# Optimization experiments

Measured on AMD Instinct MI355X. Metric: run time of the kernel, lower is better.

The kernel has to match this reference:

```python
import jax, jax.numpy as jnp
import numpy as np

B, T, K = 1024, 512, 64
START, STOP = K - 2, K - 1
NEG = -10000.0


def setup_inputs() -> dict:
    key = jax.random.key(0)
    k1, k2, k3, k4 = jax.random.split(key, 4)
    feats = jax.random.normal(k1, (B, T, K), dtype=jnp.float32)
    lengths = jax.random.randint(k2, (B,), 1, T + 1)  # valid seq lengths in [1, T]
    tags = jax.random.randint(k3, (B, T), 0, K)
    transitions = jax.random.normal(k4, (K, K), dtype=jnp.float32)
    # CRF constraints: nothing transitions INTO start, nothing transitions OUT of stop
    transitions = transitions.at[START, :].set(NEG).at[:, STOP].set(NEG)
    return {"feats": feats, "lengths": lengths, "tags": tags, "transitions": transitions}


def _forward_alg(feats, transitions, lengths):
    Bn, Tn, Kn = feats.shape
    alpha0 = jnp.full((Bn, Kn), NEG, feats.dtype).at[:, START].set(0.0)

    def step(alpha, emit):  # alpha: [B,K] over prev tag j; emit: [B,K] over cur tag i
        # tag_var[b,i,j] = emit[b,i] + trans[i,j] + alpha[b,j]
        new = jax.nn.logsumexp(emit[:, :, None] + transitions[None, :, :] + alpha[:, None, :], axis=2)
        return new, new

    _, ys = jax.lax.scan(step, alpha0, jnp.swapaxes(feats, 0, 1))  # ys: [T,B,K]
    all_alpha = jnp.concatenate([alpha0[None], ys], axis=0)  # [T+1,B,K]
    sel = all_alpha[lengths, jnp.arange(Bn)]  # alpha after `lengths` steps: [B,K]
    terminal = sel + transitions[STOP][None, :]
    return jax.nn.logsumexp(terminal, axis=1)  # [B]


def _score_sentence(feats, transitions, lengths, tags):
    Bn, Tn, Kn = feats.shape
    pad_start = jnp.concatenate([jnp.full((Bn, 1), START, tags.dtype), tags], axis=1)  # [B,T+1]
    pad_stop = jnp.concatenate([tags, jnp.full((Bn, 1), STOP, tags.dtype)], axis=1)  # [B,T+1]
    pos = jnp.arange(Tn + 1)[None, :]
    pad_stop = jnp.where(pos >= lengths[:, None], STOP, pad_stop)  # tags[lengths:] -> STOP
    trans_vals = transitions[pad_stop, pad_start]  # [B,T+1]
    trans_score = jnp.sum(jnp.where(pos <= lengths[:, None], trans_vals, 0.0), axis=1)
    emit_vals = jnp.take_along_axis(feats, tags[:, :, None], axis=2)[:, :, 0]  # [B,T]
    emit_mask = jnp.arange(Tn)[None, :] < lengths[:, None]
    emit_score = jnp.sum(jnp.where(emit_mask, emit_vals, 0.0), axis=1)
    return trans_score + emit_score


def reference(feats, lengths, tags, transitions):
    forward_score = _forward_alg(feats, transitions, lengths)
    gold_score = _score_sentence(feats, transitions, lengths, tags)
    return jnp.mean(forward_score - gold_score)
```

## Files before the change

kernel.cpp:

```cpp
#include <hip/hip_runtime.h>

#define CRF_B 1024
#define CRF_T 512
#define CRF_K 64
#define CRF_START 62
#define CRF_STOP 63

typedef float vf16 __attribute__((ext_vector_type(16)));

__device__ __forceinline__ float bcastf(float v, int lane) {
  return __int_as_float(__builtin_amdgcn_readlane(__float_as_int(v), lane));
}

__device__ __forceinline__ float wave_sum64(float v) {
#pragma unroll
  for (int off = 32; off > 0; off >>= 1) v += __shfl_xor(v, off, 64);
  return v;
}

__global__ __launch_bounds__(128, 1) void crf_kernel(
    const float* __restrict__ feats, const int* __restrict__ lengths,
    const int* __restrict__ tags, const float* __restrict__ trans,
    float* __restrict__ out) {
  __shared__ float sT[CRF_K * 65];
  __shared__ float sP[CRF_K];

  const int b = blockIdx.x;
  const int tid = threadIdx.x;
  const int lane = tid & 63;

  for (int idx = tid; idx < CRF_K * CRF_K; idx += 128)
    sT[(idx >> 6) * 65 + (idx & 63)] = trans[idx];
  __syncthreads();

  const int L = lengths[b];

  if (tid < 64) {
    vf16 E0, E1, E2, E3;
    {
      const float* trow = &sT[lane * 65];
#pragma unroll
      for (int j = 0; j < 16; ++j) E0[j] = __expf(trow[j]);
#pragma unroll
      for (int j = 0; j < 16; ++j) E1[j] = __expf(trow[16 + j]);
#pragma unroll
      for (int j = 0; j < 16; ++j) E2[j] = __expf(trow[32 + j]);
#pragma unroll
      for (int j = 0; j < 16; ++j) E3[j] = __expf(trow[48 + j]);
    }

    const float* bfeats = feats + (size_t)b * CRF_T * CRF_K + lane;

    float P = (lane == CRF_START) ? 1.0f : 0.0f;
    float offset = 0.0f;

    float e[8], f[8];
#pragma unroll
    for (int r = 0; r < 8; ++r) e[r] = bfeats[r * CRF_K];

    auto do_step = [&](float ee) {
      sP[lane] = P;
      const float4* sp4 = (const float4*)sP;
      float a0 = 0.f, a1 = 0.f, a2 = 0.f, a3 = 0.f;
#pragma unroll
      for (int jp = 0; jp < 16; ++jp) {
        float4 q = sp4[jp];
        float e0, e1, e2, e3;
        if (jp < 4) {
          e0 = E0[4 * jp]; e1 = E0[4 * jp + 1]; e2 = E0[4 * jp + 2]; e3 = E0[4 * jp + 3];
        } else if (jp < 8) {
          e0 = E1[4 * jp - 16]; e1 = E1[4 * jp - 15]; e2 = E1[4 * jp - 14]; e3 = E1[4 * jp - 13];
        } else if (jp < 12) {
          e0 = E2[4 * jp - 32]; e1 = E2[4 * jp - 31]; e2 = E2[4 * jp - 30]; e3 = E2[4 * jp - 29];
        } else {
          e0 = E3[4 * jp - 48]; e1 = E3[4 * jp - 47]; e2 = E3[4 * jp - 46]; e3 = E3[4 * jp - 45];
        }
        a0 = __builtin_fmaf(e0, q.x, a0);
        a1 = __builtin_fmaf(e1, q.y, a1);
        a2 = __builtin_fmaf(e2, q.z, a2);
        if (jp < 15) a3 = __builtin_fmaf(e3, q.w, a3);
      }
      P = ((a0 + a1) + (a2 + a3)) * ee;
    };

    auto rescale = [&](int first) {
      float M = first ? 1.0f : bcastf(P, 0);
      offset += __logf(M);
      P *= __builtin_amdgcn_rcpf(M);
    };

    const int Lb = L & ~7;
    for (int t0 = 0; t0 < Lb; t0 += 8) {
      const int tn = t0 + 8;
      if (tn < CRF_T) {
#pragma unroll
        for (int r = 0; r < 8; ++r) f[r] = bfeats[(tn + r) * CRF_K];
      } else {
#pragma unroll
        for (int r = 0; r < 8; ++r) f[r] = 0.0f;
      }
      float ee[8];
#pragma unroll
      for (int r = 0; r < 8; ++r) ee[r] = __expf(e[r]);

      rescale(t0 == 0);

#pragma unroll
      for (int r = 0; r < 8; ++r) do_step(ee[r]);
#pragma unroll
      for (int r = 0; r < 8; ++r) e[r] = f[r];
    }
    if (Lb < L) {
      rescale(Lb == 0);
#pragma unroll
      for (int r = 0; r < 8; ++r)
        if (Lb + r < L) do_step(__expf(e[r]));
    }

    float eST = __expf(sT[CRF_STOP * 65 + lane]);
    float s2 = wave_sum64(P * eST);
    float fwd = offset + __logf(s2);
    if (lane == 0) atomicAdd(out, fwd * (1.0f / CRF_B));
  } else {
    const int* btags = tags + b * CRF_T;
    const float* bf = feats + (size_t)b * CRF_T * CRF_K;
    float gold = 0.0f;
#pragma unroll
    for (int base = 0; base < CRF_T; base += 64) {
      int t = base + lane;
      if (t < L) {
        int tg = btags[t];
        int tp = (t == 0) ? CRF_START : btags[t - 1];
        gold += bf[(size_t)t * CRF_K + tg];
        gold += sT[tg * 65 + tp];
      }
    }
    gold = wave_sum64(gold);
    if (lane == 0) {
      gold += sT[CRF_STOP * 65 + btags[L - 1]];
      atomicAdd(out, -gold * (1.0f / CRF_B));
    }
  }
}

extern "C" void kernel_launch(void* const* d_in, const int* in_sizes, int n_in,
                              void* d_out, int out_size, void* d_ws, size_t ws_size,
                              hipStream_t stream) {
  const float* feats = (const float*)d_in[0];
  const int* lengths = (const int*)d_in[1];
  const int* tags = (const int*)d_in[2];
  const float* trans = (const float*)d_in[3];
  float* out = (float*)d_out;
  hipMemsetAsync(out, 0, sizeof(float), stream);
  crf_kernel<<<CRF_B, 128, 0, stream>>>(feats, lengths, tags, trans, out);
}
```

Measured before the change: 322.3 us.

## Merge gold-score and forward waves into single-wave block, drop shared transition copy

Shrinks each block to one wavefront that computes the gold path score before the forward recursion, and reads transitions straight from global memory instead of staging a padded copy in shared memory. It also preloads all 16 float4 values of the shared alpha vector into registers before the FMA chain in each step. The aim is to cut per-block LDS use, the barrier, and the extra wave, which should let more blocks sit on each CU, and to give the compiler independent LDS loads to overlap. In exchange, the gold-score work now runs serially ahead of the recursion on the same wave, and the added registers may reduce occupancy.

```diff
diff --git a/kernel.cpp b/kernel.cpp
--- a/kernel.cpp
+++ b/kernel.cpp
@@ -18,128 +18,118 @@
   return v;
 }
 
-__global__ __launch_bounds__(128, 1) void crf_kernel(
+__global__ __launch_bounds__(64, 1) void crf_kernel(
     const float* __restrict__ feats, const int* __restrict__ lengths,
     const int* __restrict__ tags, const float* __restrict__ trans,
     float* __restrict__ out) {
-  __shared__ float sT[CRF_K * 65];
   __shared__ float sP[CRF_K];
 
   const int b = blockIdx.x;
-  const int tid = threadIdx.x;
-  const int lane = tid & 63;
-
-  for (int idx = tid; idx < CRF_K * CRF_K; idx += 128)
-    sT[(idx >> 6) * 65 + (idx & 63)] = trans[idx];
-  __syncthreads();
-
+  const int lane = threadIdx.x;
   const int L = lengths[b];
 
-  if (tid < 64) {
-    vf16 E0, E1, E2, E3;
-    {
-      const float* trow = &sT[lane * 65];
+  const float* trow = trans + lane * CRF_K;
+  vf16 E0, E1, E2, E3;
 #pragma unroll
-      for (int j = 0; j < 16; ++j) E0[j] = __expf(trow[j]);
+  for (int j = 0; j < 16; ++j) E0[j] = __expf(trow[j]);
 #pragma unroll
-      for (int j = 0; j < 16; ++j) E1[j] = __expf(trow[16 + j]);
+  for (int j = 0; j < 16; ++j) E1[j] = __expf(trow[16 + j]);
 #pragma unroll
-      for (int j = 0; j < 16; ++j) E2[j] = __expf(trow[32 + j]);
+  for (int j = 0; j < 16; ++j) E2[j] = __expf(trow[32 + j]);
 #pragma unroll
-      for (int j = 0; j < 16; ++j) E3[j] = __expf(trow[48 + j]);
+  for (int j = 0; j < 16; ++j) E3[j] = __expf(trow[48 + j]);
+
+  const int* btags = tags + b * CRF_T;
+  const float* bf = feats + (size_t)b * CRF_T * CRF_K;
+  float gold = 0.0f;
+#pragma unroll
+  for (int base = 0; base < CRF_T; base += 64) {
+    int t = base + lane;
+    if (t < L) {
+      int tg = btags[t];
+      int tp = (t == 0) ? CRF_START : btags[t - 1];
+      gold += bf[(size_t)t * CRF_K + tg];
+      gold += trans[tg * CRF_K + tp];
     }
+  }
+  gold = wave_sum64(gold);
 
-    const float* bfeats = feats + (size_t)b * CRF_T * CRF_K + lane;
+  const float* bfeats = bf + lane;
+  float P = (lane == CRF_START) ? 1.0f : 0.0f;
+  float offset = 0.0f;
 
-    float P = (lane == CRF_START) ? 1.0f : 0.0f;
-    float offset = 0.0f;
+  float e[8], f[8];
+#pragma unroll
+  for (int r = 0; r < 8; ++r) e[r] = bfeats[r * CRF_K];
 
-    float e[8], f[8];
+  auto do_step = [&](float ee) {
+    sP[lane] = P;
+    const float4* sp4 = (const float4*)sP;
+    float4 q[16];
 #pragma unroll
-    for (int r = 0; r < 8; ++r) e[r] = bfeats[r * CRF_K];
+    for (int jp = 0; jp < 16; ++jp) q[jp] = sp4[jp];
+    float a0 = 0.f, a1 = 0.f, a2 = 0.f, a3 = 0.f;
+#pragma unroll
+    for (int jp = 0; jp < 16; ++jp) {
+      float e0, e1, e2, e3;
+      if (jp < 4) {
+        e0 = E0[4 * jp]; e1 = E0[4 * jp + 1]; e2 = E0[4 * jp + 2]; e3 = E0[4 * jp + 3];
+      } else if (jp < 8) {
+        e0 = E1[4 * jp - 16]; e1 = E1[4 * jp - 15]; e2 = E1[4 * jp - 14]; e3 = E1[4 * jp - 13];
+      } else if (jp < 12) {
+        e0 = E2[4 * jp - 32]; e1 = E2[4 * jp - 31]; e2 = E2[4 * jp - 30]; e3 = E2[4 * jp - 29];
+      } else {
+        e0 = E3[4 * jp - 48]; e1 = E3[4 * jp - 47]; e2 = E3[4 * jp - 46]; e3 = E3[4 * jp - 45];
+      }
+      a0 = __builtin_fmaf(e0, q[jp].x, a0);
+      a1 = __builtin_fmaf(e1, q[jp].y, a1);
+      a2 = __builtin_fmaf(e2, q[jp].z, a2);
+      if (jp < 15) a3 = __builtin_fmaf(e3, q[jp].w, a3);
+    }
+    P = ((a0 + a1) + (a2 + a3)) * ee;
+  };
 
-    auto do_step = [&](float ee) {
-      sP[lane] = P;
-      const float4* sp4 = (const float4*)sP;
-      float a0 = 0.f, a1 = 0.f, a2 = 0.f, a3 = 0.f;
+  auto rescale = [&](int first) {
+    float M = first ? 1.0f : bcastf(P, 0);
+    offset += __logf(M);
+    P *= __builtin_amdgcn_rcpf(M);
+  };
+
+  const int Lb = L & ~7;
+  for (int t0 = 0; t0 < Lb; t0 += 8) {
+    const int tn = t0 + 8;
+    if (tn < CRF_T) {
 #pragma unroll
-      for (int jp = 0; jp < 16; ++jp) {
-        float4 q = sp4[jp];
-        float e0, e1, e2, e3;
-        if (jp < 4) {
-          e0 = E0[4 * jp]; e1 = E0[4 * jp + 1]; e2 = E0[4 * jp + 2]; e3 = E0[4 * jp + 3];
-        } else if (jp < 8) {
-          e0 = E1[4 * jp - 16]; e1 = E1[4 * jp - 15]; e2 = E1[4 * jp - 14]; e3 = E1[4 * jp - 13];
-        } else if (jp < 12) {
-          e0 = E2[4 * jp - 32]; e1 = E2[4 * jp - 31]; e2 = E2[4 * jp - 30]; e3 = E2[4 * jp - 29];
-        } else {
-          e0 = E3[4 * jp - 48]; e1 = E3[4 * jp - 47]; e2 = E3[4 * jp - 46]; e3 = E3[4 * jp - 45];
-        }
-        a0 = __builtin_fmaf(e0, q.x, a0);
-        a1 = __builtin_fmaf(e1, q.y, a1);
-        a2 = __builtin_fmaf(e2, q.z, a2);
-        if (jp < 15) a3 = __builtin_fmaf(e3, q.w, a3);
-      }
-      P = ((a0 + a1) + (a2 + a3)) * ee;
-    };
+      for (int r = 0; r < 8; ++r) f[r] = bfeats[(tn + r) * CRF_K];
+    } else {
+#pragma unroll
+      for (int r = 0; r < 8; ++r) f[r] = 0.0f;
+    }
+    float ee[8];
+#pragma unroll
+    for (int r = 0; r < 8; ++r) ee[r] = __expf(e[r]);
 
-    auto rescale = [&](int first) {
-      float M = first ? 1.0f : bcastf(P, 0);
-      offset += __logf(M);
-      P *= __builtin_amdgcn_rcpf(M);
-    };
-
-    const int Lb = L & ~7;
-    for (int t0 = 0; t0 < Lb; t0 += 8) {
-      const int tn = t0 + 8;
-      if (tn < CRF_T) {
-#pragma unroll
-        for (int r = 0; r < 8; ++r) f[r] = bfeats[(tn + r) * CRF_K];
-      } else {
-#pragma unroll
-        for (int r = 0; r < 8; ++r) f[r] = 0.0f;
-      }
-      float ee[8];
-#pragma unroll
-      for (int r = 0; r < 8; ++r) ee[r] = __expf(e[r]);
-
-      rescale(t0 == 0);
+    rescale(t0 == 0);
 
 #pragma unroll
-      for (int r = 0; r < 8; ++r) do_step(ee[r]);
+    for (int r = 0; r < 8; ++r) do_step(ee[r]);
 #pragma unroll
-      for (int r = 0; r < 8; ++r) e[r] = f[r];
-    }
-    if (Lb < L) {
-      rescale(Lb == 0);
+    for (int r = 0; r < 8; ++r) e[r] = f[r];
+  }
+  if (Lb < L) {
+    rescale(Lb == 0);
 #pragma unroll
-      for (int r = 0; r < 8; ++r)
-        if (Lb + r < L) do_step(__expf(e[r]));
-    }
+    for (int r = 0; r < 8; ++r)
+      if (Lb + r < L) do_step(__expf(e[r]));
+  }
 
-    float eST = __expf(sT[CRF_STOP * 65 + lane]);
-    float s2 = wave_sum64(P * eST);
-    float fwd = offset + __logf(s2);
-    if (lane == 0) atomicAdd(out, fwd * (1.0f / CRF_B));
-  } else {
-    const int* btags = tags + b * CRF_T;
-    const float* bf = feats + (size_t)b * CRF_T * CRF_K;
-    float gold = 0.0f;
-#pragma unroll
-    for (int base = 0; base < CRF_T; base += 64) {
-      int t = base + lane;
-      if (t < L) {
-        int tg = btags[t];
-        int tp = (t == 0) ? CRF_START : btags[t - 1];
-        gold += bf[(size_t)t * CRF_K + tg];
-        gold += sT[tg * 65 + tp];
-      }
-    }
-    gold = wave_sum64(gold);
-    if (lane == 0) {
-      gold += sT[CRF_STOP * 65 + btags[L - 1]];
-      atomicAdd(out, -gold * (1.0f / CRF_B));
-    }
+  float eST = __expf(trans[CRF_STOP * CRF_K + lane]);
+  float s2 = wave_sum64(P * eST);
+  float fwd = offset + __logf(s2);
+
+  if (lane == 0) {
+    gold += trans[CRF_STOP * CRF_K + btags[L - 1]];
+    atomicAdd(out, (fwd - gold) * (1.0f / CRF_B));
   }
 }
 
@@ -152,5 +142,5 @@
   const float* trans = (const float*)d_in[3];
   float* out = (float*)d_out;
   hipMemsetAsync(out, 0, sizeof(float), stream);
-  crf_kernel<<<CRF_B, 128, 0, stream>>>(feats, lengths, tags, trans, out);
+  crf_kernel<<<CRF_B, 64, 0, stream>>>(feats, lengths, tags, trans, out);
 }
```

Result: faster. 314.4 us (-2.4%).
